# Kernel optimization log

Measured on AMD Instinct MI355X. Metric: run time of the kernel, lower is better.

## Reference

```python
import jax, jax.numpy as jnp
import numpy as np

NUM_CELLS = 8
NEIGHBORHOOD = 2.0
H_DIM = 64
ATT_DIM = 32
EMBED_DIM = 4
NUM_PED = 2048
NUM_POINTS = 8192


def setup_inputs() -> dict:
    key = jax.random.key(0)
    ks = jax.random.split(key, 12)
    s = 0.05
    return {
        "scene_info": jax.random.normal(ks[0], (NUM_POINTS, 2), jnp.float32) * 2.0,
        "curr_end_pos": jax.random.normal(ks[1], (NUM_PED, 2), jnp.float32) * 2.0,
        "curr_disp_pos": jax.random.normal(ks[2], (NUM_PED, 2), jnp.float32) * 0.1,
        "curr_hidden_1": jax.random.normal(ks[3], (NUM_PED, H_DIM), jnp.float32),
        "W_enc": jax.random.normal(ks[4], (1, ATT_DIM), jnp.float32) * s,
        "b_enc": jnp.zeros((ATT_DIM,), jnp.float32),
        "W_dec": jax.random.normal(ks[5], (H_DIM, ATT_DIM), jnp.float32) * s,
        "b_dec": jnp.zeros((ATT_DIM,), jnp.float32),
        "W_full": jax.random.normal(ks[6], (ATT_DIM, 1), jnp.float32) * s,
        "b_full": jnp.zeros((1,), jnp.float32),
        "W_fbeta": jax.random.normal(ks[7], (H_DIM, 1), jnp.float32) * s,
        "b_fbeta": jnp.zeros((1,), jnp.float32),
        "W_emb": jax.random.normal(ks[8], (4, EMBED_DIM), jnp.float32) * s,
        "b_emb": jnp.zeros((EMBED_DIM,), jnp.float32),
        "W_ih": jax.random.normal(ks[9], (EMBED_DIM + 1, 4 * H_DIM), jnp.float32) * s,
        "b_ih": jnp.zeros((4 * H_DIM,), jnp.float32),
        "W_hh": jax.random.normal(ks[10], (H_DIM, 4 * H_DIM), jnp.float32) * s,
        "b_hh": jnp.zeros((4 * H_DIM,), jnp.float32),
        "num_ped": NUM_PED,
    }


def _occupancy_grid(scene_info, curr_end_pos, num_ped):
    """Per-pedestrian occupancy grid via bounds-check + scatter_add. -> [N, G*G, 1]"""
    G = NUM_CELLS
    total = G * G
    half = NEIGHBORHOOD / 2.0
    px, py = curr_end_pos[:, 0], curr_end_pos[:, 1]          # [N]
    tlx, tly = px - half, py + half                          # top-left
    brx, bry = px + half, py - half                          # bottom-right
    sx, sy = scene_info[:, 0], scene_info[:, 1]              # [P]
    # [N, P] grid cell ids (same math as torch: floor in float, +1, +per-ped offset)
    cell_x = jnp.floor((sx[None, :] - tlx[:, None]) / NEIGHBORHOOD * G)
    cell_y = jnp.floor((tly[:, None] - sy[None, :]) / NEIGHBORHOOD * G)
    grid_pos = cell_x + cell_y * G + 1.0
    grid_pos = grid_pos + (jnp.arange(num_ped, dtype=jnp.float32) * total)[:, None]
    # torch: x_bound/y_bound are OR-ed 'outside' predicates; outside -> slot 0 (dropped)
    outside = ((sx[None, :] >= brx[:, None]) | (sx[None, :] <= tlx[:, None]) |
               (sy[None, :] >= tly[:, None]) | (sy[None, :] <= bry[:, None]))
    idx = jnp.where(outside, 0.0, grid_pos).astype(jnp.int32).reshape(-1)
    counts = jax.ops.segment_sum(
        jnp.ones(idx.shape[0], jnp.float32), idx, num_segments=num_ped * total + 1)
    return counts[1:].reshape(num_ped, total, 1)


def _attention_decoder(encoder_out, h, embed_info,
                       W_enc, b_enc, W_dec, b_dec, W_full, b_full,
                       W_fbeta, b_fbeta, W_emb, b_emb, W_ih, b_ih, W_hh, b_hh):
    # Show-Attend-Tell style additive attention over grid cells
    att1 = encoder_out @ W_enc + b_enc                       # [N, total, ATT]
    att2 = h @ W_dec + b_dec                                 # [N, ATT]
    att = (jax.nn.relu(att1 + att2[:, None, :]) @ W_full + b_full)[..., 0]  # [N, total]
    alpha = jax.nn.softmax(att, axis=1)
    awe = jnp.sum(encoder_out * alpha[..., None], axis=1)    # [N, 1]
    gate = jax.nn.sigmoid(h @ W_fbeta + b_fbeta)             # [N, 1]
    awe = gate * awe
    emb = embed_info @ W_emb + b_emb                         # [N, EMBED_DIM]
    x = jnp.concatenate([emb, awe], axis=1)                  # [N, EMBED_DIM+1]
    # LSTMCell step with (h0=h, c0=0), torch gate order i,f,g,o
    gates = x @ W_ih + b_ih + h @ W_hh + b_hh                # [N, 4H]
    i, f, g, o = jnp.split(gates, 4, axis=1)
    c = jax.nn.sigmoid(i) * jnp.tanh(g)
    return jax.nn.sigmoid(o) * jnp.tanh(c)


def reference(scene_info, curr_end_pos, curr_disp_pos, curr_hidden_1,
              W_enc, b_enc, W_dec, b_dec, W_full, b_full, W_fbeta, b_fbeta,
              W_emb, b_emb, W_ih, b_ih, W_hh, b_hh, num_ped):
    h = curr_hidden_1.reshape(-1, H_DIM)
    embed_info = jnp.concatenate([curr_end_pos, curr_disp_pos], axis=1)  # [N, 4]
    encoder_out = _occupancy_grid(scene_info, curr_end_pos, num_ped)
    curr_pool_h = _attention_decoder(encoder_out, h, embed_info,
                                     W_enc, b_enc, W_dec, b_dec, W_full, b_full,
                                     W_fbeta, b_fbeta, W_emb, b_emb,
                                     W_ih, b_ih, W_hh, b_hh)
    return curr_pool_h
```

## Files before the change

### kernel.cpp

```cpp
#include <hip/hip_runtime.h>


constexpr int CELLS = 64;
constexpr int HD    = 64;
constexpr int AD    = 32;
constexpr int PPB   = 4;
constexpr int BLK   = 512;

__global__ __launch_bounds__(BLK) void fused_ssfe_kernel(
    const float* __restrict__ scene,
    const float* __restrict__ end_pos,
    const float* __restrict__ disp_pos,
    const float* __restrict__ h_in,
    const float* __restrict__ W_enc,
    const float* __restrict__ b_enc,
    const float* __restrict__ W_dec,
    const float* __restrict__ b_dec,
    const float* __restrict__ W_full,
    const float* __restrict__ b_full,
    const float* __restrict__ W_fbeta,
    const float* __restrict__ b_fbeta,
    const float* __restrict__ W_emb,
    const float* __restrict__ b_emb,
    const float* __restrict__ W_ih,
    const float* __restrict__ b_ih,
    const float* __restrict__ W_hh,
    const float* __restrict__ b_hh,
    float* __restrict__ out,
    int nped, int npts)
{
    __shared__ unsigned hist[PPB][CELLS];
    __shared__ float    h_s[PPB][HD];
    __shared__ float    att2_s[PPB][AD];
    __shared__ float    gate_s[PPB];
    __shared__ float    x_s[PPB][8];
    __shared__ float    part[PPB][3][HD];

    const int tid  = threadIdx.x;
    const int ped0 = blockIdx.x * PPB;

    if (tid < PPB * CELLS) ((unsigned*)hist)[tid] = 0u;

    if (tid < PPB * HD) {
        int p = tid >> 6, k = tid & 63;
        int ped = ped0 + p;
        h_s[p][k] = (ped < nped) ? h_in[ped * HD + k] : 0.f;
    }

    float tlx[PPB], tly[PPB], brx[PPB], bry[PPB];
    #pragma unroll
    for (int p = 0; p < PPB; ++p) {
        float px, py;
        int ped = ped0 + p;
        if (ped < nped) { px = end_pos[ped * 2]; py = end_pos[ped * 2 + 1]; }
        else            { px = 1e30f;            py = 1e30f; }
        tlx[p] = px - 1.0f; tly[p] = py + 1.0f;
        brx[p] = px + 1.0f; bry[p] = py - 1.0f;
    }
    __syncthreads();

    auto test_point = [&](float sx, float sy) {
        #pragma unroll
        for (int p = 0; p < PPB; ++p) {
            bool outside = (sx >= brx[p]) | (sx <= tlx[p]) |
                           (sy >= tly[p]) | (sy <= bry[p]);
            if (!outside) {
                float cx = floorf((sx - tlx[p]) * 4.0f);
                float cy = floorf((tly[p] - sy) * 4.0f);
                int cell = (int)(cx + cy * 8.0f);
                atomicAdd(&hist[p][cell], 1u);
            }
        }
    };

    const float4* sc4 = reinterpret_cast<const float4*>(scene);
    const int n4 = npts >> 1;
    #pragma unroll 4
    for (int i = tid; i < n4; i += BLK) {
        float4 s = sc4[i];
        test_point(s.x, s.y);
        test_point(s.z, s.w);
    }
    if (npts & 1) {
        if (tid == 0) test_point(scene[(npts - 1) * 2], scene[(npts - 1) * 2 + 1]);
    }
    __syncthreads();

    const int wave = tid >> 6;
    const int lane = tid & 63;
    const int p    = wave & 3;
    const int half = wave >> 2;
    const int ped  = ped0 + p;

    if (half == 0) {
        if (lane < AD && ped < nped) {
            float a = b_dec[lane];
            #pragma unroll 8
            for (int k = 0; k < HD; ++k) a = fmaf(h_s[p][k], W_dec[k * AD + lane], a);
            att2_s[p][lane] = a;
        }
    } else {
        if (ped < nped) {
            float gp = h_s[p][lane] * W_fbeta[lane];
            #pragma unroll
            for (int off = 32; off; off >>= 1) gp += __shfl_xor(gp, off, 64);
            if (lane == 0) gate_s[p] = 1.f / (1.f + __expf(-(gp + b_fbeta[0])));
        }
    }
    __syncthreads();

    if (half == 0 && ped < nped) {
        float cnt = (float)hist[p][lane];
        float att = b_full[0];
        #pragma unroll 8
        for (int j = 0; j < AD; ++j) {
            float s = fmaf(cnt, W_enc[j], b_enc[j] + att2_s[p][j]);
            att = fmaf(fmaxf(s, 0.f), W_full[j], att);
        }
        float m = att;
        #pragma unroll
        for (int off = 32; off; off >>= 1) m = fmaxf(m, __shfl_xor(m, off, 64));
        float e = __expf(att - m);
        float ssum = e;
        #pragma unroll
        for (int off = 32; off; off >>= 1) ssum += __shfl_xor(ssum, off, 64);
        float awe = cnt * e / ssum;
        #pragma unroll
        for (int off = 32; off; off >>= 1) awe += __shfl_xor(awe, off, 64);

        if (lane < 4) {
            float ex = end_pos[ped * 2], ey = end_pos[ped * 2 + 1];
            float dx = disp_pos[ped * 2], dy = disp_pos[ped * 2 + 1];
            x_s[p][lane] = ex * W_emb[0 * 4 + lane] + ey * W_emb[1 * 4 + lane]
                         + dx * W_emb[2 * 4 + lane] + dy * W_emb[3 * 4 + lane]
                         + b_emb[lane];
        }
        if (lane == 4) x_s[p][4] = gate_s[p] * awe;
    }
    __syncthreads();

    if (ped < nped) {
        float acc_i, acc_g, acc_o;
        if (half == 0) {
            acc_i = b_ih[lane]       + b_hh[lane];
            acc_g = b_ih[128 + lane] + b_hh[128 + lane];
            acc_o = b_ih[192 + lane] + b_hh[192 + lane];
            #pragma unroll
            for (int k = 0; k < 5; ++k) {
                float xk = x_s[p][k];
                acc_i = fmaf(xk, W_ih[k * 256 + lane],       acc_i);
                acc_g = fmaf(xk, W_ih[k * 256 + 128 + lane], acc_g);
                acc_o = fmaf(xk, W_ih[k * 256 + 192 + lane], acc_o);
            }
        } else {
            acc_i = 0.f; acc_g = 0.f; acc_o = 0.f;
        }
        const int k0 = half * 32;
        #pragma unroll 8
        for (int k = k0; k < k0 + 32; ++k) {
            float hk = h_s[p][k];
            acc_i = fmaf(hk, W_hh[k * 256 + lane],       acc_i);
            acc_g = fmaf(hk, W_hh[k * 256 + 128 + lane], acc_g);
            acc_o = fmaf(hk, W_hh[k * 256 + 192 + lane], acc_o);
        }
        if (half == 1) {
            part[p][0][lane] = acc_i;
            part[p][1][lane] = acc_g;
            part[p][2][lane] = acc_o;
        }
        __syncthreads();
        if (half == 0) {
            acc_i += part[p][0][lane];
            acc_g += part[p][1][lane];
            acc_o += part[p][2][lane];
            float sig_i = 1.f / (1.f + __expf(-acc_i));
            float sig_o = 1.f / (1.f + __expf(-acc_o));
            float cc = sig_i * tanhf(acc_g);
            out[ped * HD + lane] = sig_o * tanhf(cc);
        }
    } else {
        __syncthreads();
    }
}

extern "C" void kernel_launch(void* const* d_in, const int* in_sizes, int n_in,
                              void* d_out, int out_size, void* d_ws, size_t ws_size,
                              hipStream_t stream)
{
    const float* scene   = (const float*)d_in[0];
    const float* end_pos = (const float*)d_in[1];
    const float* disp    = (const float*)d_in[2];
    const float* h_in    = (const float*)d_in[3];
    const float* W_enc   = (const float*)d_in[4];
    const float* b_enc   = (const float*)d_in[5];
    const float* W_dec   = (const float*)d_in[6];
    const float* b_dec   = (const float*)d_in[7];
    const float* W_full  = (const float*)d_in[8];
    const float* b_full  = (const float*)d_in[9];
    const float* W_fbeta = (const float*)d_in[10];
    const float* b_fbeta = (const float*)d_in[11];
    const float* W_emb   = (const float*)d_in[12];
    const float* b_emb   = (const float*)d_in[13];
    const float* W_ih    = (const float*)d_in[14];
    const float* b_ih    = (const float*)d_in[15];
    const float* W_hh    = (const float*)d_in[16];
    const float* b_hh    = (const float*)d_in[17];
    float* out = (float*)d_out;

    const int nped = in_sizes[1] / 2;
    const int npts = in_sizes[0] / 2;
    const int blocks = (nped + PPB - 1) / PPB;

    hipLaunchKernelGGL(fused_ssfe_kernel, dim3(blocks), dim3(BLK), 0, stream,
        scene, end_pos, disp, h_in, W_enc, b_enc, W_dec, b_dec, W_full, b_full,
        W_fbeta, b_fbeta, W_emb, b_emb, W_ih, b_ih, W_hh, b_hh, out, nped, npts);
}
```

Baseline: 18.37 us.

## Bin scene points into spatial grid so each pedestrian scans only nearby bins

Adds a single-block pre-pass that counting-sorts scene points into a 32x32 uniform grid over [-8,8]^2, clamping outliers into the edge bins, and writes bin offsets to workspace. The main kernel then has each pedestrian's two waves scan only the bin rows overlapping its 2x2 neighborhood instead of testing all 8192 points against all four pedestrians. This removes the O(N*P) brute-force bounds test. In exchange it adds a second launch and a serial single-block sort, and the per-pedestrian scan work can be uneven. It also splits the W_dec matvec across all 64 lanes and folds b_enc into att2.

```diff
diff --git a/kernel.cpp b/kernel.cpp
--- a/kernel.cpp
+++ b/kernel.cpp
@@ -7,8 +7,62 @@
 constexpr int PPB   = 4;
 constexpr int BLK   = 512;
 
+constexpr int   GB   = 32;
+constexpr int   NB   = GB * GB;
+constexpr float EXT  = 8.0f;
+constexpr float BINV = 2.0f;
+
+__device__ __forceinline__ int bin1d(float x) {
+    int b = (int)floorf((x + EXT) * BINV);
+    return min(max(b, 0), GB - 1);
+}
+
+__global__ __launch_bounds__(1024) void bin_points_kernel(
+    const float* __restrict__ scene, int npts,
+    float2* __restrict__ pts_out, unsigned* __restrict__ bin_start)
+{
+    __shared__ unsigned cnt[NB];
+    __shared__ unsigned bufA[NB], bufB[NB];
+    const int tid = threadIdx.x;
+
+    cnt[tid] = 0u;
+    __syncthreads();
+
+    const float2* sc2 = reinterpret_cast<const float2*>(scene);
+    for (int i = tid; i < npts; i += 1024) {
+        float2 s = sc2[i];
+        atomicAdd(&cnt[bin1d(s.y) * GB + bin1d(s.x)], 1u);
+    }
+    __syncthreads();
+
+    unsigned own = cnt[tid];
+    bufA[tid] = own;
+    __syncthreads();
+    unsigned* src = bufA; unsigned* dst = bufB;
+    for (int off = 1; off < NB; off <<= 1) {
+        unsigned v = src[tid];
+        if (tid >= off) v += src[tid - off];
+        dst[tid] = v;
+        __syncthreads();
+        unsigned* t = src; src = dst; dst = t;
+    }
+    unsigned incl = src[tid];
+    bin_start[tid + 1] = incl;
+    if (tid == 0) bin_start[0] = 0u;
+
+    cnt[tid] = incl - own;
+    __syncthreads();
+
+    for (int i = tid; i < npts; i += 1024) {
+        float2 s = sc2[i];
+        unsigned slot = atomicAdd(&cnt[bin1d(s.y) * GB + bin1d(s.x)], 1u);
+        pts_out[slot] = s;
+    }
+}
+
 __global__ __launch_bounds__(BLK) void fused_ssfe_kernel(
-    const float* __restrict__ scene,
+    const float2* __restrict__ pts,
+    const unsigned* __restrict__ bin_start,
     const float* __restrict__ end_pos,
     const float* __restrict__ disp_pos,
     const float* __restrict__ h_in,
@@ -27,7 +81,7 @@
     const float* __restrict__ W_hh,
     const float* __restrict__ b_hh,
     float* __restrict__ out,
-    int nped, int npts)
+    int nped)
 {
     __shared__ unsigned hist[PPB][CELLS];
     __shared__ float    h_s[PPB][HD];
@@ -38,66 +92,61 @@
 
     const int tid  = threadIdx.x;
     const int ped0 = blockIdx.x * PPB;
-
-    if (tid < PPB * CELLS) ((unsigned*)hist)[tid] = 0u;
-
-    if (tid < PPB * HD) {
-        int p = tid >> 6, k = tid & 63;
-        int ped = ped0 + p;
-        h_s[p][k] = (ped < nped) ? h_in[ped * HD + k] : 0.f;
-    }
-
-    float tlx[PPB], tly[PPB], brx[PPB], bry[PPB];
-    #pragma unroll
-    for (int p = 0; p < PPB; ++p) {
-        float px, py;
-        int ped = ped0 + p;
-        if (ped < nped) { px = end_pos[ped * 2]; py = end_pos[ped * 2 + 1]; }
-        else            { px = 1e30f;            py = 1e30f; }
-        tlx[p] = px - 1.0f; tly[p] = py + 1.0f;
-        brx[p] = px + 1.0f; bry[p] = py - 1.0f;
-    }
-    __syncthreads();
-
-    auto test_point = [&](float sx, float sy) {
-        #pragma unroll
-        for (int p = 0; p < PPB; ++p) {
-            bool outside = (sx >= brx[p]) | (sx <= tlx[p]) |
-                           (sy >= tly[p]) | (sy <= bry[p]);
-            if (!outside) {
-                float cx = floorf((sx - tlx[p]) * 4.0f);
-                float cy = floorf((tly[p] - sy) * 4.0f);
-                int cell = (int)(cx + cy * 8.0f);
-                atomicAdd(&hist[p][cell], 1u);
-            }
-        }
-    };
-
-    const float4* sc4 = reinterpret_cast<const float4*>(scene);
-    const int n4 = npts >> 1;
-    #pragma unroll 4
-    for (int i = tid; i < n4; i += BLK) {
-        float4 s = sc4[i];
-        test_point(s.x, s.y);
-        test_point(s.z, s.w);
-    }
-    if (npts & 1) {
-        if (tid == 0) test_point(scene[(npts - 1) * 2], scene[(npts - 1) * 2 + 1]);
-    }
-    __syncthreads();
-
     const int wave = tid >> 6;
     const int lane = tid & 63;
     const int p    = wave & 3;
     const int half = wave >> 2;
     const int ped  = ped0 + p;
 
+    if (tid < PPB * CELLS) ((unsigned*)hist)[tid] = 0u;
+    if (tid < PPB * HD) {
+        int pp = tid >> 6, k = tid & 63;
+        int pd = ped0 + pp;
+        h_s[pp][k] = (pd < nped) ? h_in[pd * HD + k] : 0.f;
+    }
+
+    float px, py;
+    if (ped < nped) { px = end_pos[ped * 2]; py = end_pos[ped * 2 + 1]; }
+    else            { px = 1e30f;            py = 1e30f; }
+    const float tlx = px - 1.0f, tly = py + 1.0f;
+    const float brx = px + 1.0f, bry = py - 1.0f;
+    __syncthreads();
+
+    {
+        const int bx0 = bin1d(tlx), bx1 = bin1d(brx);
+        const int by0 = bin1d(bry), by1 = bin1d(tly);
+        const unsigned lo = (unsigned)(half * 64 + lane);
+        for (int by = by0; by <= by1; ++by) {
+            const int rb = by * GB;
+            const unsigned s = bin_start[rb + bx0];
+            const unsigned e = bin_start[rb + bx1 + 1];
+            for (unsigned i = s + lo; i < e; i += 128u) {
+                float2 pt = pts[i];
+                bool outside = (pt.x >= brx) | (pt.x <= tlx) |
+                               (pt.y >= tly) | (pt.y <= bry);
+                if (!outside) {
+                    float cx = floorf((pt.x - tlx) * 4.0f);
+                    float cy = floorf((tly - pt.y) * 4.0f);
+                    int cell = (int)(cx + cy * 8.0f);
+                    atomicAdd(&hist[p][cell], 1u);
+                }
+            }
+        }
+    }
+    __syncthreads();
+
     if (half == 0) {
-        if (lane < AD && ped < nped) {
-            float a = b_dec[lane];
+        if (ped < nped) {
+            const int col   = lane & 31;
+            const int kbase = (lane >> 5) * 32;
+            float a = 0.f;
             #pragma unroll 8
-            for (int k = 0; k < HD; ++k) a = fmaf(h_s[p][k], W_dec[k * AD + lane], a);
-            att2_s[p][lane] = a;
+            for (int k = 0; k < 32; ++k) {
+                int kk = kbase + k;
+                a = fmaf(h_s[p][kk], W_dec[kk * AD + col], a);
+            }
+            a += __shfl_xor(a, 32, 64);
+            if (lane < AD) att2_s[p][lane] = a + b_dec[lane] + b_enc[lane];
         }
     } else {
         if (ped < nped) {
@@ -114,7 +163,7 @@
         float att = b_full[0];
         #pragma unroll 8
         for (int j = 0; j < AD; ++j) {
-            float s = fmaf(cnt, W_enc[j], b_enc[j] + att2_s[p][j]);
+            float s = fmaf(cnt, W_enc[j], att2_s[p][j]);
             att = fmaf(fmaxf(s, 0.f), W_full[j], att);
         }
         float m = att;
@@ -209,9 +258,16 @@
 
     const int nped = in_sizes[1] / 2;
     const int npts = in_sizes[0] / 2;
+
+    float2*   pts_ws  = (float2*)d_ws;
+    unsigned* bins_ws = (unsigned*)((char*)d_ws + (size_t)npts * sizeof(float2));
+
+    hipLaunchKernelGGL(bin_points_kernel, dim3(1), dim3(1024), 0, stream,
+        scene, npts, pts_ws, bins_ws);
+
     const int blocks = (nped + PPB - 1) / PPB;
-
     hipLaunchKernelGGL(fused_ssfe_kernel, dim3(blocks), dim3(BLK), 0, stream,
-        scene, end_pos, disp, h_in, W_enc, b_enc, W_dec, b_dec, W_full, b_full,
-        W_fbeta, b_fbeta, W_emb, b_emb, W_ih, b_ih, W_hh, b_hh, out, nped, npts);
-}
+        pts_ws, bins_ws, end_pos, disp, h_in, W_enc, b_enc, W_dec, b_dec,
+        W_full, b_full, W_fbeta, b_fbeta, W_emb, b_emb, W_ih, b_ih, W_hh, b_hh,
+        out, nped);
+}
```

Measured after the change: 26.01 us. 41.5% more time.

## Halve pedestrians per block and restructure the post-histogram phases

Applied to the files above, without the earlier changes.

Drops to 2 pedestrians and 256 threads per block, doubling the grid so more blocks can be resident. Removes two barriers by merging the attention, gate, embedding and LSTM input stages into a single wave per pedestrian. The second wave computes half of the W_hh product in parallel. Sigmoid and tanh now use hardware reciprocal approximations. The cost is that every block still reads the full 8192-point scene, so total scene traffic and point tests double, and the fast math slightly changes numerics.

```diff
diff --git a/kernel.cpp b/kernel.cpp
--- a/kernel.cpp
+++ b/kernel.cpp
@@ -4,10 +4,18 @@
 constexpr int CELLS = 64;
 constexpr int HD    = 64;
 constexpr int AD    = 32;
-constexpr int PPB   = 4;
-constexpr int BLK   = 512;
-
-__global__ __launch_bounds__(BLK) void fused_ssfe_kernel(
+constexpr int PPB   = 2;
+constexpr int BLK   = 256;
+
+__device__ __forceinline__ float fsig(float x) {
+    return __builtin_amdgcn_rcpf(1.f + __expf(-x));
+}
+__device__ __forceinline__ float ftanh(float x) {
+    float e = __expf(2.f * x);
+    return 1.f - 2.f * __builtin_amdgcn_rcpf(e + 1.f);
+}
+
+__global__ __launch_bounds__(BLK, 4) void fused_ssfe_kernel(
     const float* __restrict__ scene,
     const float* __restrict__ end_pos,
     const float* __restrict__ disp_pos,
@@ -32,89 +40,103 @@
     __shared__ unsigned hist[PPB][CELLS];
     __shared__ float    h_s[PPB][HD];
     __shared__ float    att2_s[PPB][AD];
-    __shared__ float    gate_s[PPB];
-    __shared__ float    x_s[PPB][8];
     __shared__ float    part[PPB][3][HD];
 
     const int tid  = threadIdx.x;
     const int ped0 = blockIdx.x * PPB;
-
-    if (tid < PPB * CELLS) ((unsigned*)hist)[tid] = 0u;
-
-    if (tid < PPB * HD) {
-        int p = tid >> 6, k = tid & 63;
-        int ped = ped0 + p;
-        h_s[p][k] = (ped < nped) ? h_in[ped * HD + k] : 0.f;
-    }
-
-    float tlx[PPB], tly[PPB], brx[PPB], bry[PPB];
-    #pragma unroll
-    for (int p = 0; p < PPB; ++p) {
-        float px, py;
-        int ped = ped0 + p;
-        if (ped < nped) { px = end_pos[ped * 2]; py = end_pos[ped * 2 + 1]; }
-        else            { px = 1e30f;            py = 1e30f; }
-        tlx[p] = px - 1.0f; tly[p] = py + 1.0f;
-        brx[p] = px + 1.0f; bry[p] = py - 1.0f;
-    }
-    __syncthreads();
-
-    auto test_point = [&](float sx, float sy) {
-        #pragma unroll
-        for (int p = 0; p < PPB; ++p) {
-            bool outside = (sx >= brx[p]) | (sx <= tlx[p]) |
-                           (sy >= tly[p]) | (sy <= bry[p]);
-            if (!outside) {
-                float cx = floorf((sx - tlx[p]) * 4.0f);
-                float cy = floorf((tly[p] - sy) * 4.0f);
-                int cell = (int)(cx + cy * 8.0f);
-                atomicAdd(&hist[p][cell], 1u);
-            }
-        }
-    };
-
-    const float4* sc4 = reinterpret_cast<const float4*>(scene);
-    const int n4 = npts >> 1;
-    #pragma unroll 4
-    for (int i = tid; i < n4; i += BLK) {
-        float4 s = sc4[i];
-        test_point(s.x, s.y);
-        test_point(s.z, s.w);
-    }
-    if (npts & 1) {
-        if (tid == 0) test_point(scene[(npts - 1) * 2], scene[(npts - 1) * 2 + 1]);
-    }
-    __syncthreads();
-
     const int wave = tid >> 6;
     const int lane = tid & 63;
-    const int p    = wave & 3;
-    const int half = wave >> 2;
+    const int p    = wave & 1;
+    const int half = wave >> 1;
     const int ped  = ped0 + p;
 
-    if (half == 0) {
-        if (lane < AD && ped < nped) {
-            float a = b_dec[lane];
+    if (tid < PPB * CELLS) ((unsigned*)hist)[tid] = 0u;
+    if (tid < PPB * HD) {
+        int pp = tid >> 6, k = tid & 63;
+        int pd = ped0 + pp;
+        h_s[pp][k] = (pd < nped) ? h_in[pd * HD + k] : 0.f;
+    }
+
+    float px0, py0, px1, py1;
+    px0 = end_pos[ped0 * 2 + 0]; py0 = end_pos[ped0 * 2 + 1];
+    if (ped0 + 1 < nped) { px1 = end_pos[ped0 * 2 + 2]; py1 = end_pos[ped0 * 2 + 3]; }
+    else                 { px1 = 1e30f;                 py1 = 1e30f; }
+    const float tlx0 = px0 - 1.0f, tly0 = py0 + 1.0f, brx0 = px0 + 1.0f, bry0 = py0 - 1.0f;
+    const float tlx1 = px1 - 1.0f, tly1 = py1 + 1.0f, brx1 = px1 + 1.0f, bry1 = py1 - 1.0f;
+    __syncthreads();
+
+    {
+        const float4* sc4 = reinterpret_cast<const float4*>(scene);
+        const int n4 = npts >> 1;
+        #pragma unroll 4
+        for (int i = tid; i < n4; i += BLK) {
+            float4 s = sc4[i];
+            {
+                bool o = (s.x >= brx0) | (s.x <= tlx0) | (s.y >= tly0) | (s.y <= bry0);
+                if (!o) {
+                    int c = (int)(floorf((s.x - tlx0) * 4.f) + floorf((tly0 - s.y) * 4.f) * 8.f);
+                    atomicAdd(&hist[0][c], 1u);
+                }
+            }
+            {
+                bool o = (s.x >= brx1) | (s.x <= tlx1) | (s.y >= tly1) | (s.y <= bry1);
+                if (!o) {
+                    int c = (int)(floorf((s.x - tlx1) * 4.f) + floorf((tly1 - s.y) * 4.f) * 8.f);
+                    atomicAdd(&hist[1][c], 1u);
+                }
+            }
+            {
+                bool o = (s.z >= brx0) | (s.z <= tlx0) | (s.w >= tly0) | (s.w <= bry0);
+                if (!o) {
+                    int c = (int)(floorf((s.z - tlx0) * 4.f) + floorf((tly0 - s.w) * 4.f) * 8.f);
+                    atomicAdd(&hist[0][c], 1u);
+                }
+            }
+            {
+                bool o = (s.z >= brx1) | (s.z <= tlx1) | (s.w >= tly1) | (s.w <= bry1);
+                if (!o) {
+                    int c = (int)(floorf((s.z - tlx1) * 4.f) + floorf((tly1 - s.w) * 4.f) * 8.f);
+                    atomicAdd(&hist[1][c], 1u);
+                }
+            }
+        }
+    }
+    __syncthreads();
+
+    float acc_i, acc_g, acc_o;
+
+    if (half == 1) {
+        if (ped < nped) {
+            acc_i = 0.f; acc_g = 0.f; acc_o = 0.f;
             #pragma unroll 8
-            for (int k = 0; k < HD; ++k) a = fmaf(h_s[p][k], W_dec[k * AD + lane], a);
-            att2_s[p][lane] = a;
-        }
-    } else {
-        if (ped < nped) {
-            float gp = h_s[p][lane] * W_fbeta[lane];
-            #pragma unroll
-            for (int off = 32; off; off >>= 1) gp += __shfl_xor(gp, off, 64);
-            if (lane == 0) gate_s[p] = 1.f / (1.f + __expf(-(gp + b_fbeta[0])));
-        }
-    }
-    __syncthreads();
-
-    if (half == 0 && ped < nped) {
+            for (int k = 32; k < 64; ++k) {
+                float hk = h_s[p][k];
+                acc_i = fmaf(hk, W_hh[k * 256 + lane],       acc_i);
+                acc_g = fmaf(hk, W_hh[k * 256 + 128 + lane], acc_g);
+                acc_o = fmaf(hk, W_hh[k * 256 + 192 + lane], acc_o);
+            }
+            part[p][0][lane] = acc_i;
+            part[p][1][lane] = acc_g;
+            part[p][2][lane] = acc_o;
+        }
+    } else if (ped < nped) {
+        {
+            const int col   = lane & 31;
+            const int kbase = (lane >> 5) * 32;
+            float a = 0.f;
+            #pragma unroll 8
+            for (int k = 0; k < 32; ++k) {
+                int kk = kbase + k;
+                a = fmaf(h_s[p][kk], W_dec[kk * AD + col], a);
+            }
+            a += __shfl_xor(a, 32, 64);
+            if (lane < AD) att2_s[p][lane] = a + b_dec[lane] + b_enc[lane];
+        }
         float cnt = (float)hist[p][lane];
         float att = b_full[0];
         #pragma unroll 8
         for (int j = 0; j < AD; ++j) {
-            float s = fmaf(cnt, W_enc[j], b_enc[j] + att2_s[p][j]);
+            float s = fmaf(cnt, W_enc[j], att2_s[p][j]);
             att = fmaf(fmaxf(s, 0.f), W_full[j], att);
         }
         float m = att;
@@ -124,62 +146,58 @@
         float ssum = e;
         #pragma unroll
         for (int off = 32; off; off >>= 1) ssum += __shfl_xor(ssum, off, 64);
-        float awe = cnt * e / ssum;
+        float awe = cnt * e * __builtin_amdgcn_rcpf(ssum);
         #pragma unroll
         for (int off = 32; off; off >>= 1) awe += __shfl_xor(awe, off, 64);
 
-        if (lane < 4) {
-            float ex = end_pos[ped * 2], ey = end_pos[ped * 2 + 1];
-            float dx = disp_pos[ped * 2], dy = disp_pos[ped * 2 + 1];
-            x_s[p][lane] = ex * W_emb[0 * 4 + lane] + ey * W_emb[1 * 4 + lane]
-                         + dx * W_emb[2 * 4 + lane] + dy * W_emb[3 * 4 + lane]
-                         + b_emb[lane];
-        }
-        if (lane == 4) x_s[p][4] = gate_s[p] * awe;
-    }
-    __syncthreads();
-
-    if (ped < nped) {
-        float acc_i, acc_g, acc_o;
-        if (half == 0) {
-            acc_i = b_ih[lane]       + b_hh[lane];
-            acc_g = b_ih[128 + lane] + b_hh[128 + lane];
-            acc_o = b_ih[192 + lane] + b_hh[192 + lane];
-            #pragma unroll
-            for (int k = 0; k < 5; ++k) {
-                float xk = x_s[p][k];
-                acc_i = fmaf(xk, W_ih[k * 256 + lane],       acc_i);
-                acc_g = fmaf(xk, W_ih[k * 256 + 128 + lane], acc_g);
-                acc_o = fmaf(xk, W_ih[k * 256 + 192 + lane], acc_o);
-            }
-        } else {
-            acc_i = 0.f; acc_g = 0.f; acc_o = 0.f;
-        }
-        const int k0 = half * 32;
+        float gp = h_s[p][lane] * W_fbeta[lane];
+        #pragma unroll
+        for (int off = 32; off; off >>= 1) gp += __shfl_xor(gp, off, 64);
+        float gate = fsig(gp + b_fbeta[0]);
+        float aweg = gate * awe;
+
+        float dx = disp_pos[ped * 2], dy = disp_pos[ped * 2 + 1];
+        float ex = (p == 0) ? px0 : px1;
+        float ey = (p == 0) ? py0 : py1;
+        float x0 = ex * W_emb[0]  + ey * W_emb[4]  + dx * W_emb[8]  + dy * W_emb[12] + b_emb[0];
+        float x1 = ex * W_emb[1]  + ey * W_emb[5]  + dx * W_emb[9]  + dy * W_emb[13] + b_emb[1];
+        float x2 = ex * W_emb[2]  + ey * W_emb[6]  + dx * W_emb[10] + dy * W_emb[14] + b_emb[2];
+        float x3 = ex * W_emb[3]  + ey * W_emb[7]  + dx * W_emb[11] + dy * W_emb[15] + b_emb[3];
+
+        acc_i = b_ih[lane]       + b_hh[lane];
+        acc_g = b_ih[128 + lane] + b_hh[128 + lane];
+        acc_o = b_ih[192 + lane] + b_hh[192 + lane];
+        acc_i = fmaf(x0, W_ih[0 * 256 + lane], acc_i);
+        acc_g = fmaf(x0, W_ih[0 * 256 + 128 + lane], acc_g);
+        acc_o = fmaf(x0, W_ih[0 * 256 + 192 + lane], acc_o);
+        acc_i = fmaf(x1, W_ih[1 * 256 + lane], acc_i);
+        acc_g = fmaf(x1, W_ih[1 * 256 + 128 + lane], acc_g);
+        acc_o = fmaf(x1, W_ih[1 * 256 + 192 + lane], acc_o);
+        acc_i = fmaf(x2, W_ih[2 * 256 + lane], acc_i);
+        acc_g = fmaf(x2, W_ih[2 * 256 + 128 + lane], acc_g);
+        acc_o = fmaf(x2, W_ih[2 * 256 + 192 + lane], acc_o);
+        acc_i = fmaf(x3, W_ih[3 * 256 + lane], acc_i);
+        acc_g = fmaf(x3, W_ih[3 * 256 + 128 + lane], acc_g);
+        acc_o = fmaf(x3, W_ih[3 * 256 + 192 + lane], acc_o);
+        acc_i = fmaf(aweg, W_ih[4 * 256 + lane], acc_i);
+        acc_g = fmaf(aweg, W_ih[4 * 256 + 128 + lane], acc_g);
+        acc_o = fmaf(aweg, W_ih[4 * 256 + 192 + lane], acc_o);
         #pragma unroll 8
-        for (int k = k0; k < k0 + 32; ++k) {
+        for (int k = 0; k < 32; ++k) {
             float hk = h_s[p][k];
             acc_i = fmaf(hk, W_hh[k * 256 + lane],       acc_i);
             acc_g = fmaf(hk, W_hh[k * 256 + 128 + lane], acc_g);
             acc_o = fmaf(hk, W_hh[k * 256 + 192 + lane], acc_o);
         }
-        if (half == 1) {
-            part[p][0][lane] = acc_i;
-            part[p][1][lane] = acc_g;
-            part[p][2][lane] = acc_o;
-        }
-        __syncthreads();
-        if (half == 0) {
-            acc_i += part[p][0][lane];
-            acc_g += part[p][1][lane];
-            acc_o += part[p][2][lane];
-            float sig_i = 1.f / (1.f + __expf(-acc_i));
-            float sig_o = 1.f / (1.f + __expf(-acc_o));
-            float cc = sig_i * tanhf(acc_g);
-            out[ped * HD + lane] = sig_o * tanhf(cc);
-        }
-    } else {
-        __syncthreads();
+    }
+    __syncthreads();
+
+    if (half == 0 && ped < nped) {
+        acc_i += part[p][0][lane];
+        acc_g += part[p][1][lane];
+        acc_o += part[p][2][lane];
+        float cc = fsig(acc_i) * ftanh(acc_g);
+        out[ped * HD + lane] = fsig(acc_o) * ftanh(cc);
     }
 }
 
```

After: 17.44 us. 5.1% less time.
